# Performance work log

Hardware: AMD Instinct MI355X
Metric: run time of the kernel (lower is better)

The kernel has to match this reference:

```python
import jax, jax.numpy as jnp
import numpy as np


def setup_inputs() -> dict:
    key = jax.random.key(0)
    k1, k2, k3 = jax.random.split(key, 3)
    B, C, S, Fin, Fout = 16, 64, 2048, 64, 64
    x = jax.random.normal(k1, (B, C, S, Fin), dtype=jnp.float32)
    # positive entries so row sums are > 0 and sqrt is well-defined
    adj = jax.random.uniform(k2, (C, C), dtype=jnp.float32)
    weight = jax.random.normal(k3, (Fin, Fout), dtype=jnp.float32) * (1.0 / np.sqrt(Fin))
    return {"x": x, "adj": adj, "weight": weight}


def reference(x, adj, weight):
    # Symmetric normalization: D^{-1/2} A D^{-1/2}. The torch code builds a
    # full diag + matrix inverse; mathematically this is elementwise rsqrt
    # row/col scaling of adj.
    d_inv_sqrt = jax.lax.rsqrt(jnp.sum(adj, axis=1))          # [C]
    norm_adj = adj * d_inv_sqrt[:, None] * d_inv_sqrt[None, :]  # [C, C]
    # support[b,c,s,o] = sum_f x[b,c,s,f] * weight[f,o]
    support = jnp.einsum('bcsf,fo->bcso', x, weight)
    # mix over channel (graph node) dim: out[b,c,s,o] = sum_d A_norm[c,d] support[b,d,s,o]
    out = jnp.einsum('cd,bdso->bcso', norm_adj, support)
    return jax.nn.relu(out)
```

## Files before the change

### kernel.cpp

```cpp
#include <hip/hip_runtime.h>
#include <hip/hip_bf16.h>

#define B_ 16
#define C_ 64
#define S_ 2048
#define F_ 64
#define SF (S_ * F_)

typedef __attribute__((ext_vector_type(8))) short short8;
typedef __attribute__((ext_vector_type(4))) float float4_;

__device__ __forceinline__ unsigned short f2bf(float f) {
    unsigned int u = __builtin_bit_cast(unsigned int, f);
    u += 0x7fffu + ((u >> 16) & 1u);
    return (unsigned short)(u >> 16);
}

__global__ void gcn_prep(const float* __restrict__ adj, const float* __restrict__ wgt,
                         unsigned short* __restrict__ nadj, unsigned short* __restrict__ wT)
{
    __shared__ float dis[C_];
    const int t = threadIdx.x;
    if (t < C_) {
        float s = 0.f;
        for (int d = 0; d < C_; ++d) s += adj[t * C_ + d];
        dis[t] = rsqrtf(s);
    }
    __syncthreads();
    for (int i = t; i < C_ * C_; i += 256) {
        const int c = i >> 6, d = i & 63;
        nadj[i] = f2bf(adj[i] * dis[c] * dis[d]);
        wT[d * F_ + c] = f2bf(wgt[i]);
    }
}

__global__ __launch_bounds__(512) void gcn_main(
    const float* __restrict__ x,
    const unsigned short* __restrict__ nadj,
    const unsigned short* __restrict__ wT,
    float* __restrict__ out)
{
    __shared__ unsigned short supT[8 * 64 * 64];

    const int tid  = threadIdx.x;
    const int w    = tid >> 6;
    const int l    = tid & 63;
    const int lrow = l & 15;
    const int lgrp = l >> 4;

    const int b  = blockIdx.x >> 8;
    const int st = blockIdx.x & 255;
    const int s  = st * 8 + w;

    short8 wf[4][2];
#pragma unroll
    for (int ot = 0; ot < 4; ++ot)
#pragma unroll
        for (int ks = 0; ks < 2; ++ks)
            wf[ot][ks] = *(const short8*)(wT + (ot * 16 + lrow) * 64 + ks * 32 + lgrp * 8);

    const float* xb = x + (size_t)b * C_ * SF + (size_t)s * F_;
    short8 af[4][2];
#pragma unroll
    for (int dt = 0; dt < 4; ++dt) {
        const float* xr = xb + (size_t)(dt * 16 + lrow) * SF;
#pragma unroll
        for (int ks = 0; ks < 2; ++ks) {
            float4_ u0 = *(const float4_*)(xr + ks * 32 + lgrp * 8);
            float4_ u1 = *(const float4_*)(xr + ks * 32 + lgrp * 8 + 4);
            short8 a;
#pragma unroll
            for (int j = 0; j < 4; ++j) {
                a[j]     = (short)f2bf(u0[j]);
                a[4 + j] = (short)f2bf(u1[j]);
            }
            af[dt][ks] = a;
        }
    }

#pragma unroll
    for (int dt = 0; dt < 4; ++dt) {
        const int dbase = dt * 16 + lgrp * 4;
#pragma unroll
        for (int ot = 0; ot < 4; ++ot) {
            float4_ acc = {0.f, 0.f, 0.f, 0.f};
            acc = __builtin_amdgcn_mfma_f32_16x16x32_bf16(af[dt][0], wf[ot][0], acc, 0, 0, 0);
            acc = __builtin_amdgcn_mfma_f32_16x16x32_bf16(af[dt][1], wf[ot][1], acc, 0, 0, 0);
            const int n = w * 64 + ot * 16 + lrow;
            const int e = n * 64 + (dbase ^ ((n & 7) << 3));
            uint2 pk;
            pk.x = (unsigned)f2bf(acc[0]) | ((unsigned)f2bf(acc[1]) << 16);
            pk.y = (unsigned)f2bf(acc[2]) | ((unsigned)f2bf(acc[3]) << 16);
            *(uint2*)(supT + e) = pk;
        }
    }

    short8 bfr[4][2];
#pragma unroll
    for (int ot = 0; ot < 4; ++ot) {
        const int n = w * 64 + ot * 16 + lrow;
#pragma unroll
        for (int ks = 0; ks < 2; ++ks) {
            const int e = n * 64 + ((ks * 32 + lgrp * 8) ^ ((n & 7) << 3));
            bfr[ot][ks] = *(const short8*)(supT + e);
        }
    }

    float* ob = out + (size_t)b * C_ * SF + (size_t)s * F_;
#pragma unroll
    for (int ct = 0; ct < 4; ++ct) {
        short8 an[2];
#pragma unroll
        for (int ks = 0; ks < 2; ++ks)
            an[ks] = *(const short8*)(nadj + (ct * 16 + lrow) * 64 + ks * 32 + lgrp * 8);
        const int cb = ct * 16 + lgrp * 4;
#pragma unroll
        for (int ot = 0; ot < 4; ++ot) {
            float4_ acc = {0.f, 0.f, 0.f, 0.f};
            acc = __builtin_amdgcn_mfma_f32_16x16x32_bf16(an[0], bfr[ot][0], acc, 0, 0, 0);
            acc = __builtin_amdgcn_mfma_f32_16x16x32_bf16(an[1], bfr[ot][1], acc, 0, 0, 0);
            const int o = ot * 16 + lrow;
#pragma unroll
            for (int i = 0; i < 4; ++i)
                ob[(size_t)(cb + i) * SF + o] = fmaxf(acc[i], 0.f);
        }
    }
}

extern "C" void kernel_launch(void* const* d_in, const int* in_sizes, int n_in,
                              void* d_out, int out_size, void* d_ws, size_t ws_size,
                              hipStream_t stream) {
    const float* x   = (const float*)d_in[0];
    const float* adj = (const float*)d_in[1];
    const float* wgt = (const float*)d_in[2];
    float* out = (float*)d_out;

    unsigned short* nadj = (unsigned short*)d_ws;
    unsigned short* wT   = nadj + C_ * C_;

    gcn_prep<<<1, 256, 0, stream>>>(adj, wgt, nadj, wT);

    dim3 grid(B_ * (S_ / 8));
    gcn_main<<<grid, 512, 0, stream>>>(x, nadj, wT, out);
}
```

Baseline: 265.3 us.

## Stage adjacency and weights in swizzled LDS, process per output tile, vectorize stores

Copies the normalized adjacency and transposed weight into swizzled LDS once per block instead of each wave loading them from global memory. The work is restructured to loop over output-feature tiles: each tile's support slice goes into a smaller per-wave LDS buffer and is consumed right away, which cuts LDS use. The second MFMA swaps operands so each lane writes four contiguous floats with a single 16-byte store instead of four strided scalar stores. It also adds a minimum-blocks hint to the launch bounds and a block-wide barrier after staging.

```diff
diff --git a/kernel.cpp b/kernel.cpp
--- a/kernel.cpp
+++ b/kernel.cpp
@@ -9,6 +9,8 @@
 
 typedef __attribute__((ext_vector_type(8))) short short8;
 typedef __attribute__((ext_vector_type(4))) float float4_;
+
+#define SWZ(row, col) ((col) ^ (((row) & 7) << 3))
 
 __device__ __forceinline__ unsigned short f2bf(float f) {
     unsigned int u = __builtin_bit_cast(unsigned int, f);
@@ -34,13 +36,15 @@
     }
 }
 
-__global__ __launch_bounds__(512) void gcn_main(
+__global__ __launch_bounds__(512, 4) void gcn_main(
     const float* __restrict__ x,
     const unsigned short* __restrict__ nadj,
     const unsigned short* __restrict__ wT,
     float* __restrict__ out)
 {
-    __shared__ unsigned short supT[8 * 64 * 64];
+    __shared__ __align__(16) unsigned short lds_nadj[C_ * C_];
+    __shared__ __align__(16) unsigned short lds_wT[F_ * F_];
+    __shared__ __align__(16) unsigned short supT[8 * 16 * F_];
 
     const int tid  = threadIdx.x;
     const int w    = tid >> 6;
@@ -48,16 +52,17 @@
     const int lrow = l & 15;
     const int lgrp = l >> 4;
 
+    {
+        const int fc = tid >> 3;
+        const int fd = (tid & 7) * 8;
+        *(short8*)(lds_nadj + fc * 64 + SWZ(fc, fd)) = *(const short8*)(nadj + fc * 64 + fd);
+        *(short8*)(lds_wT  + fc * 64 + SWZ(fc, fd)) = *(const short8*)(wT  + fc * 64 + fd);
+    }
+    __syncthreads();
+
     const int b  = blockIdx.x >> 8;
     const int st = blockIdx.x & 255;
     const int s  = st * 8 + w;
-
-    short8 wf[4][2];
-#pragma unroll
-    for (int ot = 0; ot < 4; ++ot)
-#pragma unroll
-        for (int ks = 0; ks < 2; ++ks)
-            wf[ot][ks] = *(const short8*)(wT + (ot * 16 + lrow) * 64 + ks * 32 + lgrp * 8);
 
     const float* xb = x + (size_t)b * C_ * SF + (size_t)s * F_;
     short8 af[4][2];
@@ -78,51 +83,42 @@
         }
     }
 
-#pragma unroll
-    for (int dt = 0; dt < 4; ++dt) {
-        const int dbase = dt * 16 + lgrp * 4;
-#pragma unroll
-        for (int ot = 0; ot < 4; ++ot) {
-            float4_ acc = {0.f, 0.f, 0.f, 0.f};
-            acc = __builtin_amdgcn_mfma_f32_16x16x32_bf16(af[dt][0], wf[ot][0], acc, 0, 0, 0);
-            acc = __builtin_amdgcn_mfma_f32_16x16x32_bf16(af[dt][1], wf[ot][1], acc, 0, 0, 0);
-            const int n = w * 64 + ot * 16 + lrow;
-            const int e = n * 64 + (dbase ^ ((n & 7) << 3));
-            uint2 pk;
-            pk.x = (unsigned)f2bf(acc[0]) | ((unsigned)f2bf(acc[1]) << 16);
-            pk.y = (unsigned)f2bf(acc[2]) | ((unsigned)f2bf(acc[3]) << 16);
-            *(uint2*)(supT + e) = pk;
-        }
-    }
+    unsigned short* myT = supT + w * (16 * F_);
+    float* ob = out + (size_t)b * C_ * SF + (size_t)s * F_;
 
-    short8 bfr[4][2];
 #pragma unroll
     for (int ot = 0; ot < 4; ++ot) {
-        const int n = w * 64 + ot * 16 + lrow;
+        const int orow = ot * 16 + lrow;
+        short8 wf0 = *(const short8*)(lds_wT + orow * 64 + SWZ(lrow, lgrp * 8));
+        short8 wf1 = *(const short8*)(lds_wT + orow * 64 + SWZ(lrow, 32 + lgrp * 8));
+
 #pragma unroll
-        for (int ks = 0; ks < 2; ++ks) {
-            const int e = n * 64 + ((ks * 32 + lgrp * 8) ^ ((n & 7) << 3));
-            bfr[ot][ks] = *(const short8*)(supT + e);
+        for (int dt = 0; dt < 4; ++dt) {
+            float4_ s1 = {0.f, 0.f, 0.f, 0.f};
+            s1 = __builtin_amdgcn_mfma_f32_16x16x32_bf16(af[dt][0], wf0, s1, 0, 0, 0);
+            s1 = __builtin_amdgcn_mfma_f32_16x16x32_bf16(af[dt][1], wf1, s1, 0, 0, 0);
+            const int dbase = dt * 16 + lgrp * 4;
+            uint2 pk;
+            pk.x = (unsigned)f2bf(s1[0]) | ((unsigned)f2bf(s1[1]) << 16);
+            pk.y = (unsigned)f2bf(s1[2]) | ((unsigned)f2bf(s1[3]) << 16);
+            *(uint2*)(myT + lrow * 64 + SWZ(lrow, dbase)) = pk;
         }
-    }
 
-    float* ob = out + (size_t)b * C_ * SF + (size_t)s * F_;
+        short8 bf0 = *(const short8*)(myT + lrow * 64 + SWZ(lrow, lgrp * 8));
+        short8 bf1 = *(const short8*)(myT + lrow * 64 + SWZ(lrow, 32 + lgrp * 8));
+
 #pragma unroll
-    for (int ct = 0; ct < 4; ++ct) {
-        short8 an[2];
+        for (int ct = 0; ct < 4; ++ct) {
+            const int crow = ct * 16 + lrow;
+            short8 an0 = *(const short8*)(lds_nadj + crow * 64 + SWZ(lrow, lgrp * 8));
+            short8 an1 = *(const short8*)(lds_nadj + crow * 64 + SWZ(lrow, 32 + lgrp * 8));
+            float4_ acc = {0.f, 0.f, 0.f, 0.f};
+            acc = __builtin_amdgcn_mfma_f32_16x16x32_bf16(bf0, an0, acc, 0, 0, 0);
+            acc = __builtin_amdgcn_mfma_f32_16x16x32_bf16(bf1, an1, acc, 0, 0, 0);
+            float4_ r;
 #pragma unroll
-        for (int ks = 0; ks < 2; ++ks)
-            an[ks] = *(const short8*)(nadj + (ct * 16 + lrow) * 64 + ks * 32 + lgrp * 8);
-        const int cb = ct * 16 + lgrp * 4;
-#pragma unroll
-        for (int ot = 0; ot < 4; ++ot) {
-            float4_ acc = {0.f, 0.f, 0.f, 0.f};
-            acc = __builtin_amdgcn_mfma_f32_16x16x32_bf16(an[0], bfr[ot][0], acc, 0, 0, 0);
-            acc = __builtin_amdgcn_mfma_f32_16x16x32_bf16(an[1], bfr[ot][1], acc, 0, 0, 0);
-            const int o = ot * 16 + lrow;
-#pragma unroll
-            for (int i = 0; i < 4; ++i)
-                ob[(size_t)(cb + i) * SF + o] = fmaxf(acc[i], 0.f);
+            for (int i = 0; i < 4; ++i) r[i] = fmaxf(acc[i], 0.f);
+            *(float4_*)(ob + (size_t)crow * SF + ot * 16 + lgrp * 4) = r;
         }
     }
 }
```

Measured after the change: 253.5 us. 4.4% less time.
